# Optimization experiments

Measured on AMD Instinct MI355X. Metric: run time of the kernel, lower is better.

## Reference

```python
import jax, jax.numpy as jnp
from jax import lax
import numpy as np

# Bit order convention: pulse index 0 = MSB (sign bit), index 31 = LSB of mantissa.
SHIFTS = jnp.arange(31, -1, -1, dtype=jnp.uint32)  # [32]


def f32_to_pulses(x):
    """float32 [...] -> pulse bits [..., 32] in {0.,1.}"""
    u = lax.bitcast_convert_type(x.astype(jnp.float32), jnp.uint32)
    return ((u[..., None] >> SHIFTS) & jnp.uint32(1)).astype(jnp.float32)


def pulses_to_f32(p):
    """pulse bits [..., 32] -> float32 [...]"""
    bits = (p > 0.5).astype(jnp.uint32)
    u = jnp.sum(bits << SHIFTS, axis=-1).astype(jnp.uint32)
    return lax.bitcast_convert_type(u, jnp.float32)


def setup_inputs() -> dict:
    key = jax.random.key(0)
    kx, kw = jax.random.split(key)
    B, IN, OUT = 256, 1024, 1024
    x_f = jax.random.normal(kx, (B, IN), dtype=jnp.float32)
    w_f = jax.random.normal(kw, (OUT, IN), dtype=jnp.float32) * (1.0 / np.sqrt(IN))
    return {"x": f32_to_pulses(x_f), "weight_pulse": f32_to_pulses(w_f)}


def reference(x, weight_pulse):
    # Decode pulses to IEEE-754 FP32 values (exact: the spiking multiplier/adder
    # implement bit-exact FP32 arithmetic).
    xf = pulses_to_f32(x)              # [B, in]
    wf = pulses_to_f32(weight_pulse)   # [out, in]
    prods = xf[..., None, :] * wf      # [B, out, in]
    # SequentialAccumulator: strictly left-to-right FP32 accumulation (bit-exact
    # deterministic order), expressed as a scan over the in_features axis.
    acc0 = jnp.zeros(prods.shape[:-1], dtype=jnp.float32)  # [B, out]
    acc, _ = lax.scan(lambda a, p: (a + p, None), acc0, jnp.moveaxis(prods, -1, 0))
    # Re-encode the FP32 result to output pulses [B, out, 32].
    return f32_to_pulses(acc)
```

## Files before the change

kernel.cpp:

```cpp
#include <hip/hip_runtime.h>
#include <cstdint>

#define BATCH 256
#define INF   1024
#define OUTF  1024

__device__ __forceinline__ uint32_t assemble_bits(const float4* __restrict__ p4) {
    uint32_t u = 0;
#pragma unroll
    for (int j = 0; j < 8; ++j) {
        float4 v = p4[j];
        int sh = 31 - j * 4;
        u |= (v.x > 0.5f ? 1u : 0u) << sh;
        u |= (v.y > 0.5f ? 1u : 0u) << (sh - 1);
        u |= (v.z > 0.5f ? 1u : 0u) << (sh - 2);
        u |= (v.w > 0.5f ? 1u : 0u) << (sh - 3);
    }
    return u;
}

__global__ __launch_bounds__(256) void decode_pulses(
    const float* __restrict__ pulses, float* __restrict__ out, int n) {
    int i = blockIdx.x * blockDim.x + threadIdx.x;
    if (i >= n) return;
    const float4* p4 = reinterpret_cast<const float4*>(pulses) + (size_t)i * 8;
    out[i] = __uint_as_float(assemble_bits(p4));
}

__global__ __launch_bounds__(256) void decode_pulses_wT(
    const float* __restrict__ pulses, float* __restrict__ wT) {
    int i = blockIdx.x * blockDim.x + threadIdx.x;
    int o = i >> 10;
    int k = i & (INF - 1);
    const float4* p4 = reinterpret_cast<const float4*>(pulses) + (size_t)i * 8;
    wT[(size_t)k * OUTF + o] = __uint_as_float(assemble_bits(p4));
}

__global__ __launch_bounds__(256) void gemm_encode(
    const float* __restrict__ xf,
    const float* __restrict__ wT,
    float* __restrict__ out)
{
#pragma clang fp contract(off)
    int o = blockIdx.x * 64 + threadIdx.x;
    int b = blockIdx.y * 4 + threadIdx.y;

    const float* __restrict__ xrow = xf + (size_t)b * INF;
    const float* __restrict__ wcol = wT + o;

    float acc = 0.0f;
    for (int k = 0; k < INF; ++k) {
        float p = xrow[k] * wcol[(size_t)k * OUTF];
        acc = acc + p;
    }

    uint32_t u = __float_as_uint(acc);
    float4* dst = reinterpret_cast<float4*>(out) + ((size_t)b * OUTF + o) * 8;
#pragma unroll
    for (int j = 0; j < 8; ++j) {
        int sh = 31 - j * 4;
        dst[j] = make_float4((float)((u >> sh) & 1u),
                             (float)((u >> (sh - 1)) & 1u),
                             (float)((u >> (sh - 2)) & 1u),
                             (float)((u >> (sh - 3)) & 1u));
    }
}

extern "C" void kernel_launch(void* const* d_in, const int* in_sizes, int n_in,
                              void* d_out, int out_size, void* d_ws, size_t ws_size,
                              hipStream_t stream) {
    const float* x_pulses = (const float*)d_in[0];
    const float* w_pulses = (const float*)d_in[1];
    float* out = (float*)d_out;

    float* xf = (float*)d_ws;
    float* wT = xf + (size_t)BATCH * INF;

    {
        int n = BATCH * INF;
        decode_pulses<<<(n + 255) / 256, 256, 0, stream>>>(x_pulses, xf, n);
    }
    {
        int n = OUTF * INF;
        decode_pulses_wT<<<n / 256, 256, 0, stream>>>(w_pulses, wT);
    }
    {
        dim3 grid(OUTF / 64, BATCH / 4);
        dim3 block(64, 4);
        gemm_encode<<<grid, block, 0, stream>>>(xf, wT, out);
    }
}
```

Measured before the change: 291.8 us.

## Drop weight transpose, vectorize K loop, two batch rows per thread

The weight decode now writes the row-major layout with coalesced stores, replacing the transposed layout that needed scattered writes. The GEMM thread walks its weight row with float4 loads. Each thread computes two batch rows that share the same weight loads, and the grid is halved to match. Output pulses are written with nontemporal stores. The left-to-right accumulation order per output is preserved. The risk is that weight loads across lanes are now 4KB-strided instead of coalesced, which leans on cache reuse across consecutive iterations.

```diff
diff --git a/kernel.cpp b/kernel.cpp
--- a/kernel.cpp
+++ b/kernel.cpp
@@ -4,6 +4,8 @@
 #define BATCH 256
 #define INF   1024
 #define OUTF  1024
+
+typedef float floatx4 __attribute__((ext_vector_type(4)));
 
 __device__ __forceinline__ uint32_t assemble_bits(const float4* __restrict__ p4) {
     uint32_t u = 0;
@@ -27,42 +29,50 @@
     out[i] = __uint_as_float(assemble_bits(p4));
 }
 
-__global__ __launch_bounds__(256) void decode_pulses_wT(
-    const float* __restrict__ pulses, float* __restrict__ wT) {
-    int i = blockIdx.x * blockDim.x + threadIdx.x;
-    int o = i >> 10;
-    int k = i & (INF - 1);
-    const float4* p4 = reinterpret_cast<const float4*>(pulses) + (size_t)i * 8;
-    wT[(size_t)k * OUTF + o] = __uint_as_float(assemble_bits(p4));
-}
-
 __global__ __launch_bounds__(256) void gemm_encode(
     const float* __restrict__ xf,
-    const float* __restrict__ wT,
+    const float* __restrict__ wf,
     float* __restrict__ out)
 {
 #pragma clang fp contract(off)
-    int o = blockIdx.x * 64 + threadIdx.x;
-    int b = blockIdx.y * 4 + threadIdx.y;
+    const int o  = blockIdx.x * 64 + threadIdx.x;
+    const int b0 = (blockIdx.y * 4 + threadIdx.y) * 2;
 
-    const float* __restrict__ xrow = xf + (size_t)b * INF;
-    const float* __restrict__ wcol = wT + o;
+    const float4* __restrict__ w4 = reinterpret_cast<const float4*>(wf + (size_t)o * INF);
+    const float4* __restrict__ xa = reinterpret_cast<const float4*>(xf + (size_t)b0 * INF);
+    const float4* __restrict__ xb = reinterpret_cast<const float4*>(xf + (size_t)(b0 + 1) * INF);
 
-    float acc = 0.0f;
-    for (int k = 0; k < INF; ++k) {
-        float p = xrow[k] * wcol[(size_t)k * OUTF];
-        acc = acc + p;
+    float acc0 = 0.0f, acc1 = 0.0f;
+#pragma unroll 4
+    for (int kk = 0; kk < INF / 4; ++kk) {
+        float4 w = w4[kk];
+        float4 a = xa[kk];
+        float4 b = xb[kk];
+        acc0 = acc0 + a.x * w.x;
+        acc0 = acc0 + a.y * w.y;
+        acc0 = acc0 + a.z * w.z;
+        acc0 = acc0 + a.w * w.w;
+        acc1 = acc1 + b.x * w.x;
+        acc1 = acc1 + b.y * w.y;
+        acc1 = acc1 + b.z * w.z;
+        acc1 = acc1 + b.w * w.w;
     }
 
-    uint32_t u = __float_as_uint(acc);
-    float4* dst = reinterpret_cast<float4*>(out) + ((size_t)b * OUTF + o) * 8;
+    float accs[2] = {acc0, acc1};
 #pragma unroll
-    for (int j = 0; j < 8; ++j) {
-        int sh = 31 - j * 4;
-        dst[j] = make_float4((float)((u >> sh) & 1u),
-                             (float)((u >> (sh - 1)) & 1u),
-                             (float)((u >> (sh - 2)) & 1u),
-                             (float)((u >> (sh - 3)) & 1u));
+    for (int q = 0; q < 2; ++q) {
+        uint32_t u = __float_as_uint(accs[q]);
+        floatx4* dst = reinterpret_cast<floatx4*>(
+            reinterpret_cast<float*>(out) + ((size_t)(b0 + q) * OUTF + o) * 32);
+#pragma unroll
+        for (int j = 0; j < 8; ++j) {
+            int sh = 31 - j * 4;
+            floatx4 v = { (float)((u >> sh) & 1u),
+                          (float)((u >> (sh - 1)) & 1u),
+                          (float)((u >> (sh - 2)) & 1u),
+                          (float)((u >> (sh - 3)) & 1u) };
+            __builtin_nontemporal_store(v, dst + j);
+        }
     }
 }
 
@@ -74,7 +84,7 @@
     float* out = (float*)d_out;
 
     float* xf = (float*)d_ws;
-    float* wT = xf + (size_t)BATCH * INF;
+    float* wf = xf + (size_t)BATCH * INF;
 
     {
         int n = BATCH * INF;
@@ -82,11 +92,11 @@
     }
     {
         int n = OUTF * INF;
-        decode_pulses_wT<<<n / 256, 256, 0, stream>>>(w_pulses, wT);
+        decode_pulses<<<n / 256, 256, 0, stream>>>(w_pulses, wf, n);
     }
     {
-        dim3 grid(OUTF / 64, BATCH / 4);
+        dim3 grid(OUTF / 64, BATCH / 8);
         dim3 block(64, 4);
-        gemm_encode<<<grid, block, 0, stream>>>(xf, wT, out);
+        gemm_encode<<<grid, block, 0, stream>>>(xf, wf, out);
     }
 }
```

Result: slower. 375.8 us (+28.8%).

## Tile GEMM through shared memory and transpose weights via LDS tile

Applied to the files above, without the earlier changes.

The weight decode now goes through a padded 64x64 shared-memory tile, so both the pulse reads and the transposed writes are coalesced instead of scattered. The GEMM now stages 64x64 weight tiles and 8x64 input tiles in shared memory and gives each thread two batch rows, so every weight value loaded is used twice. Strict left-to-right FP32 accumulation order is kept. The cost is extra syncthreads per k-tile and more shared memory per block, with a grid half the previous size.

```diff
diff --git a/kernel.cpp b/kernel.cpp
--- a/kernel.cpp
+++ b/kernel.cpp
@@ -27,13 +27,32 @@
     out[i] = __uint_as_float(assemble_bits(p4));
 }
 
-__global__ __launch_bounds__(256) void decode_pulses_wT(
-    const float* __restrict__ pulses, float* __restrict__ wT) {
-    int i = blockIdx.x * blockDim.x + threadIdx.x;
-    int o = i >> 10;
-    int k = i & (INF - 1);
-    const float4* p4 = reinterpret_cast<const float4*>(pulses) + (size_t)i * 8;
-    wT[(size_t)k * OUTF + o] = __uint_as_float(assemble_bits(p4));
+__global__ __launch_bounds__(512) void decode_w_transpose(
+    const float* __restrict__ pulses,
+    float* __restrict__ wT)
+{
+    __shared__ float tile[64][65];
+    const int o0 = blockIdx.x * 64;
+    const int k0 = blockIdx.y * 64;
+    const int t  = threadIdx.x;
+
+    const int o_loc  = t >> 3;
+    const int k_base = t & 7;
+    const float4* src = reinterpret_cast<const float4*>(pulses)
+                        + ((size_t)(o0 + o_loc) * INF + k0 + k_base) * 8;
+#pragma unroll
+    for (int j = 0; j < 8; ++j) {
+        tile[o_loc][k_base + 8 * j] = __uint_as_float(assemble_bits(src + (size_t)(8 * j) * 8));
+    }
+    __syncthreads();
+
+    const int col = t & 63;
+    const int w   = t >> 6;
+#pragma unroll
+    for (int j2 = 0; j2 < 8; ++j2) {
+        int krow = j2 * 8 + w;
+        wT[(size_t)(k0 + krow) * OUTF + o0 + col] = tile[col][krow];
+    }
 }
 
 __global__ __launch_bounds__(256) void gemm_encode(
@@ -42,27 +61,74 @@
     float* __restrict__ out)
 {
 #pragma clang fp contract(off)
-    int o = blockIdx.x * 64 + threadIdx.x;
-    int b = blockIdx.y * 4 + threadIdx.y;
+    __shared__ float w_s[64 * 64];
+    __shared__ float x_s[8][64];
+    const int tx = threadIdx.x, ty = threadIdx.y;
+    const int t  = ty * 64 + tx;
+    const int o0 = blockIdx.x * 64;
+    const int b0 = blockIdx.y * 8;
 
-    const float* __restrict__ xrow = xf + (size_t)b * INF;
-    const float* __restrict__ wcol = wT + o;
+    const int wrow = t >> 4;
+    const int wseg = t & 15;
 
-    float acc = 0.0f;
-    for (int k = 0; k < INF; ++k) {
-        float p = xrow[k] * wcol[(size_t)k * OUTF];
-        acc = acc + p;
+    float acc0 = 0.0f, acc1 = 0.0f;
+
+    for (int kt = 0; kt < 16; ++kt) {
+        const int k0 = kt * 64;
+        __syncthreads();
+        {
+#pragma unroll
+            for (int h = 0; h < 4; ++h) {
+                float4 v = *reinterpret_cast<const float4*>(
+                    wT + (size_t)(k0 + wrow + 16 * h) * OUTF + o0 + wseg * 4);
+                *reinterpret_cast<float4*>(&w_s[(size_t)(t + 256 * h) * 4]) = v;
+            }
+        }
+        if (t < 128) {
+            int xr = t >> 4, xs = t & 15;
+            float4 v = *reinterpret_cast<const float4*>(
+                xf + (size_t)(b0 + xr) * INF + k0 + xs * 4);
+            *reinterpret_cast<float4*>(&x_s[xr][xs * 4]) = v;
+        }
+        __syncthreads();
+
+        const float* wcol  = w_s + tx;
+        const float* xrow0 = x_s[ty * 2];
+        const float* xrow1 = x_s[ty * 2 + 1];
+#pragma unroll
+        for (int k4 = 0; k4 < 16; ++k4) {
+            float4 xa = *reinterpret_cast<const float4*>(xrow0 + k4 * 4);
+            float4 xb = *reinterpret_cast<const float4*>(xrow1 + k4 * 4);
+            float w0 = wcol[(k4 * 4 + 0) * 64];
+            float w1 = wcol[(k4 * 4 + 1) * 64];
+            float w2 = wcol[(k4 * 4 + 2) * 64];
+            float w3 = wcol[(k4 * 4 + 3) * 64];
+            acc0 = acc0 + xa.x * w0;
+            acc0 = acc0 + xa.y * w1;
+            acc0 = acc0 + xa.z * w2;
+            acc0 = acc0 + xa.w * w3;
+            acc1 = acc1 + xb.x * w0;
+            acc1 = acc1 + xb.y * w1;
+            acc1 = acc1 + xb.z * w2;
+            acc1 = acc1 + xb.w * w3;
+        }
     }
 
-    uint32_t u = __float_as_uint(acc);
-    float4* dst = reinterpret_cast<float4*>(out) + ((size_t)b * OUTF + o) * 8;
+    const int o = o0 + tx;
+    float accs[2] = {acc0, acc1};
 #pragma unroll
-    for (int j = 0; j < 8; ++j) {
-        int sh = 31 - j * 4;
-        dst[j] = make_float4((float)((u >> sh) & 1u),
-                             (float)((u >> (sh - 1)) & 1u),
-                             (float)((u >> (sh - 2)) & 1u),
-                             (float)((u >> (sh - 3)) & 1u));
+    for (int q = 0; q < 2; ++q) {
+        uint32_t u = __float_as_uint(accs[q]);
+        float4* dst = reinterpret_cast<float4*>(out)
+                      + ((size_t)(b0 + ty * 2 + q) * OUTF + o) * 8;
+#pragma unroll
+        for (int j = 0; j < 8; ++j) {
+            int sh = 31 - j * 4;
+            dst[j] = make_float4((float)((u >> sh) & 1u),
+                                 (float)((u >> (sh - 1)) & 1u),
+                                 (float)((u >> (sh - 2)) & 1u),
+                                 (float)((u >> (sh - 3)) & 1u));
+        }
     }
 }
 
@@ -81,11 +147,10 @@
         decode_pulses<<<(n + 255) / 256, 256, 0, stream>>>(x_pulses, xf, n);
     }
     {
-        int n = OUTF * INF;
-        decode_pulses_wT<<<n / 256, 256, 0, stream>>>(w_pulses, wT);
+        decode_w_transpose<<<dim3(16, 16), 512, 0, stream>>>(w_pulses, wT);
     }
     {
-        dim3 grid(OUTF / 64, BATCH / 4);
+        dim3 grid(OUTF / 64, BATCH / 8);
         dim3 block(64, 4);
         gemm_encode<<<grid, block, 0, stream>>>(xf, wT, out);
     }
```

New measurement: 279.8 us. 1.04x faster.
